# Kernel optimization log

Hardware: AMD Instinct MI355X
Metric: run time of the kernel (lower is better)

The kernel has to match this reference:

```python
import jax, jax.numpy as jnp
import numpy as np

N = 1_000_000          # points
C_IN = 10              # decorated point features
C_OUT = 64             # pillar feature channels
S = 30_000             # number of pillars (segments)
EPS = 1e-3             # BatchNorm1d eps


def setup_inputs() -> dict:
    key = jax.random.key(0)
    ks = jax.random.split(key, 8)
    inputs = jax.random.normal(ks[0], (N, C_IN), dtype=jnp.float32)
    # every pillar gets ~N/S points; sorted, all segments non-empty
    unq_inv = jnp.sort(jnp.arange(N, dtype=jnp.int32) % S)
    W_lin = jax.random.normal(ks[1], (C_OUT, C_IN), dtype=jnp.float32) * 0.3
    gamma = 1.0 + 0.1 * jax.random.normal(ks[2], (C_OUT,), dtype=jnp.float32)
    beta = 0.1 * jax.random.normal(ks[3], (C_OUT,), dtype=jnp.float32)
    dw1 = jax.random.normal(ks[4], (C_OUT,), dtype=jnp.float32) * 0.5      # depthwise 1x1 conv (groups=C)
    pw1 = jax.random.normal(ks[5], (C_OUT, C_OUT), dtype=jnp.float32) * 0.1  # pointwise 1x1 conv
    dw2 = jax.random.normal(ks[6], (C_OUT,), dtype=jnp.float32) * 0.5
    pw2 = jax.random.normal(ks[7], (C_OUT, C_OUT), dtype=jnp.float32) * 0.1
    return {"inputs": inputs, "unq_inv": unq_inv, "W_lin": W_lin,
            "gamma": gamma, "beta": beta, "dw1": dw1, "pw1": pw1,
            "dw2": dw2, "pw2": pw2}


def reference(inputs, unq_inv, W_lin, gamma, beta, dw1, pw1, dw2, pw2):
    # Linear (no bias) -> BN (training-mode batch stats) -> ReLU
    x = inputs @ W_lin.T                                   # [N, C]
    mu = jnp.mean(x, axis=0)
    var = jnp.mean(jnp.square(x - mu), axis=0)             # biased var, as torch BN
    x = (x - mu) * jax.lax.rsqrt(var + EPS) * gamma + beta
    x = jax.nn.relu(x)

    # MAFF attention: local branch (depthwise scale -> swish -> 1x1 conv)
    s = x * dw1                                            # groups=C 1x1 conv == per-channel scale
    xl = (s * jax.nn.sigmoid(s)) @ pw1.T                   # [N, C]
    # global branch: avg-pool over points -> depthwise scale -> relu -> 1x1 conv
    g = jnp.mean(x, axis=0)                                # [C]
    xg = pw2 @ jax.nn.relu(dw2 * g)                        # [C]
    wei = jax.nn.sigmoid(xl + xg)                          # broadcast [N,C] + [C]
    xi = x * (1.0 + wei)

    # segment reductions keyed by pillar id (scatter_max + scatter_sum)
    x_max = jax.ops.segment_max(xi, unq_inv, num_segments=S,
                                indices_are_sorted=True)
    x_sum = jax.ops.segment_sum(xi, unq_inv, num_segments=S,
                                indices_are_sorted=True)
    return x_max + x_sum                                   # [S, C]
```

## Files before the change

### kernel.cpp

```cpp
#include <hip/hip_runtime.h>
#include <math.h>

#define N_PTS   1000000
#define CI      10
#define C       64
#define NSEG    30000
#define BN_EPS  1e-3f
#define FROFF   31104

#define MSTR 7
#define GOFF 512
#define GSTR 8
#define CTRI 961

using f32x4 = __attribute__((ext_vector_type(4))) float;
using s16x8 = __attribute__((ext_vector_type(8))) short;

__device__ inline short f2bf(float x) {
    unsigned u = __float_as_uint(x);
    unsigned r = (u + 0x7fffu + ((u >> 16) & 1u)) >> 16;
    return (short)r;
}
__device__ inline unsigned pack_trunc(float lo, float hi) {
    return (__float_as_uint(hi) & 0xffff0000u) | (__float_as_uint(lo) >> 16);
}
__device__ inline float frcp(float x) { return __builtin_amdgcn_rcpf(x); }
__device__ inline void lds_fence() {
    asm volatile("s_waitcnt lgkmcnt(0)" ::: "memory");
}

struct Rows { float2 r0, r1, r2, r3; };

__global__ void __launch_bounds__(256) k_moments(const float* __restrict__ inp,
                                                 const int* __restrict__ idx,
                                                 float* __restrict__ ws,
                                                 int* __restrict__ starts) {
    const int tid = threadIdx.x;
    const int stride = gridDim.x * blockDim.x;
    float v[65];
#pragma unroll
    for (int k = 0; k < 65; ++k) v[k] = 0.f;

    int p = blockIdx.x * blockDim.x + tid;
    float2 a0, a1, a2, a3, a4;
    int ic = 0, ip = 0;
    auto ld = [&](int qq) {
        const float2* r2 = (const float2*)(inp + (size_t)qq * CI);
        a0 = r2[0]; a1 = r2[1]; a2 = r2[2]; a3 = r2[3]; a4 = r2[4];
        ic = idx[qq]; ip = (qq > 0) ? idx[qq - 1] : ic;
    };
    if (p < N_PTS) ld(p);
    while (p < N_PTS) {
        float r[CI] = {a0.x, a0.y, a1.x, a1.y, a2.x, a2.y, a3.x, a3.y, a4.x, a4.y};
        const int cc = ic, cp = ip, cq = p;
        const int pn = p + stride;
        if (pn < N_PTS) ld(pn);

#pragma unroll
        for (int i = 0; i < CI; ++i) v[i] += r[i];
        int kk = 10;
#pragma unroll
        for (int i = 0; i < CI; ++i)
#pragma unroll
            for (int j = i; j < CI; ++j) { v[kk] = fmaf(r[i], r[j], v[kk]); ++kk; }

        if (cq == 0) starts[0] = 0;
        else if (cp != cc) starts[cc] = cq;
        p = pn;
    }

#pragma unroll
    for (int k = 0; k < 65; ++k) {
#pragma unroll
        for (int off = 32; off >= 1; off >>= 1)
            v[k] += __shfl_xor(v[k], off, 64);
    }
    __shared__ float red[4 * 65];
    const int wv = tid >> 6, ln = tid & 63;
    if (ln == 0) {
#pragma unroll
        for (int k = 0; k < 65; ++k) red[wv * 65 + k] = v[k];
    }
    __syncthreads();
    if (tid < 65)
        atomicAdd(&ws[MSTR * tid],
                  red[tid] + red[65 + tid] + red[130 + tid] + red[195 + tid]);
}

__global__ void __launch_bounds__(256) k_gstats(const float* __restrict__ inp,
                                                const float* __restrict__ W,
                                                const float* __restrict__ gamma,
                                                const float* __restrict__ beta,
                                                const float* __restrict__ dw1,
                                                const float* __restrict__ pw1,
                                                const float* __restrict__ dw2,
                                                const float* __restrict__ pw2,
                                                float* __restrict__ ws) {
    const int tid  = threadIdx.x;
    const int wv   = tid >> 6;
    const int lane = tid & 63;
    const int m = lane & 15;
    const int q = lane >> 4;

    __shared__ float wp[C * CI];
    __shared__ float bsh[C];

    if (tid < C) {
        const int c = tid;
        float w[CI];
#pragma unroll
        for (int i = 0; i < CI; ++i) w[i] = W[c * CI + i];
        const float inv_n = 1.f / (float)N_PTS;

        float mu = 0.f;
#pragma unroll
        for (int i = 0; i < CI; ++i) mu = fmaf(w[i], ws[MSTR * i], mu);
        mu *= inv_n;

        float ex2 = 0.f;
        int kk = 10;
#pragma unroll
        for (int i = 0; i < CI; ++i)
#pragma unroll
            for (int j = i; j < CI; ++j) {
                float mm = ws[MSTR * kk];
                float t = w[i] * w[j] * mm;
                ex2 += (i == j) ? t : 2.f * t;
                ++kk;
            }
        ex2 *= inv_n;

        float var = ex2 - mu * mu;
        float rstd = rsqrtf(var + BN_EPS);
        float a = rstd * gamma[c];
        float b = beta[c] - mu * a;
        bsh[c] = b;
#pragma unroll
        for (int i = 0; i < CI; ++i) wp[c * CI + i] = a * w[i];
    }
    __syncthreads();

    s16x8 wfr[4];
#pragma unroll
    for (int nt = 0; nt < 4; ++nt) {
        s16x8 t;
#pragma unroll
        for (int j = 0; j < 8; ++j) {
            int k = 8 * q + j;
            t[j] = (k < CI) ? f2bf(wp[(nt * 16 + m) * CI + k]) : (short)0;
        }
        wfr[nt] = t;
    }
    float bb[4];
#pragma unroll
    for (int nt = 0; nt < 4; ++nt) bb[nt] = bsh[nt * 16 + m];

    const int wid = blockIdx.x * 4 + wv;
    const int nw  = gridDim.x * 4;
    const int NB  = N_PTS / 16;

    auto loadrows = [&](int pb) -> Rows {
        Rows R;
        R.r0 = R.r1 = R.r2 = R.r3 = make_float2(0.f, 0.f);
        const float* row = inp + (size_t)(pb + m) * CI;
        if (q == 0) {
            R.r0 = *(const float2*)(row);     R.r1 = *(const float2*)(row + 2);
            R.r2 = *(const float2*)(row + 4); R.r3 = *(const float2*)(row + 6);
        } else if (q == 1) {
            R.r0 = *(const float2*)(row + 8);
        }
        return R;
    };

    float sm[4] = {0.f, 0.f, 0.f, 0.f};
    const f32x4 zero = {0.f, 0.f, 0.f, 0.f};

    Rows A  = loadrows(wid * 16);
    Rows Bv = loadrows((wid + nw) * 16);
    for (int b = wid; b < NB; b += nw) {
        Rows L = A; A = Bv;
        if (b + 2 * nw < NB) Bv = loadrows((b + 2 * nw) * 16);

        union { s16x8 v; unsigned u[4]; } t;
        t.v = s16x8{0, 0, 0, 0, 0, 0, 0, 0};
        if (q < 2) t.u[0] = pack_trunc(L.r0.x, L.r0.y);
        if (q == 0) {
            t.u[1] = pack_trunc(L.r1.x, L.r1.y);
            t.u[2] = pack_trunc(L.r2.x, L.r2.y);
            t.u[3] = pack_trunc(L.r3.x, L.r3.y);
        }

#pragma unroll
        for (int nt = 0; nt < 4; ++nt) {
            f32x4 xt = __builtin_amdgcn_mfma_f32_16x16x32_bf16(t.v, wfr[nt], zero, 0, 0, 0);
#pragma unroll
            for (int r = 0; r < 4; ++r)
                sm[nt] += fmaxf(xt[r] + bb[nt], 0.f);
        }
    }

#pragma unroll
    for (int nt = 0; nt < 4; ++nt) {
        sm[nt] += __shfl_xor(sm[nt], 16, 64);
        sm[nt] += __shfl_xor(sm[nt], 32, 64);
    }
    float S = sm[0];
    if (q == 1) S = sm[1];
    if (q == 2) S = sm[2];
    if (q == 3) S = sm[3];

    __shared__ float red[4 * 64];
    red[wv * 64 + lane] = S;
    __syncthreads();
    if (tid < 64)
        atomicAdd(&ws[GOFF + GSTR * tid],
                  red[tid] + red[64 + tid] + red[128 + tid] + red[192 + tid]);

    __shared__ int lastf;
    __syncthreads();
    if (tid == 0) {
        __threadfence();
        int old = atomicAdd((int*)ws + CTRI, 1);
        lastf = (old == (int)gridDim.x - 1);
    }
    __syncthreads();
    if (!lastf) return;
    __threadfence();

    __shared__ float T[C], XG[C];
    const float inv_n = 1.f / (float)N_PTS;
    if (tid < 64)
        T[tid] = fmaxf(dw2[tid] * (ws[GOFF + GSTR * tid] * inv_n), 0.f);
    __syncthreads();
    if (tid < 64) {
        float acc = 0.f;
#pragma unroll
        for (int k = 0; k < C; ++k) acc = fmaf(pw2[tid * C + k], T[k], acc);
        XG[tid] = acc;
    }
    __syncthreads();

    if (tid < 64) {
        float4* FR = (float4*)(ws + FROFF);
        union { float4 f; s16x8 v; } u;

#pragma unroll
        for (int nt = 0; nt < 4; ++nt) {
            s16x8 tt;
#pragma unroll
            for (int j = 0; j < 8; ++j) {
                int k = 8 * q + j;
                tt[j] = (k < CI) ? f2bf(wp[(nt * 16 + m) * CI + k]) : (short)0;
            }
            u.v = tt; FR[nt * 64 + lane] = u.f;
        }
#pragma unroll
        for (int nt = 0; nt < 4; ++nt)
#pragma unroll
            for (int kc = 0; kc < 2; ++kc) {
                const float* src = pw1 + (nt * 16 + m) * C + kc * 32 + q * 8;
                float4 p0 = *(const float4*)src, p1 = *(const float4*)(src + 4);
                s16x8 tt;
                tt[0] = f2bf(p0.x); tt[1] = f2bf(p0.y); tt[2] = f2bf(p0.z); tt[3] = f2bf(p0.w);
                tt[4] = f2bf(p1.x); tt[5] = f2bf(p1.y); tt[6] = f2bf(p1.z); tt[7] = f2bf(p1.w);
                u.v = tt; FR[(4 + nt * 2 + kc) * 64 + lane] = u.f;
            }
        float4 f;
        f.x = bsh[m]; f.y = bsh[16 + m]; f.z = bsh[32 + m]; f.w = bsh[48 + m];
        FR[12 * 64 + lane] = f;
        f.x = dw1[m]; f.y = dw1[16 + m]; f.z = dw1[32 + m]; f.w = dw1[48 + m];
        FR[13 * 64 + lane] = f;
        f.x = XG[m]; f.y = XG[16 + m]; f.z = XG[32 + m]; f.w = XG[48 + m];
        FR[14 * 64 + lane] = f;
    }
}

#define LD2 72
#define TILE2 (16 * LD2)
#define SEGW 2
__global__ void __launch_bounds__(256) k_main(const float* __restrict__ inp,
                                              const float* __restrict__ ws,
                                              const int* __restrict__ starts,
                                              float* __restrict__ out) {
    const int tid  = threadIdx.x;
    const int wv   = tid >> 6;
    const int lane = tid & 63;
    const int m = lane & 15;
    const int q = lane >> 4;
    const f32x4 zero = {0.f, 0.f, 0.f, 0.f};

    const float4* FR = (const float4*)(ws + FROFF);
    union { float4 f; s16x8 v; } u;
    s16x8 wfr[4];
#pragma unroll
    for (int nt = 0; nt < 4; ++nt) { u.f = FR[nt * 64 + lane]; wfr[nt] = u.v; }
    s16x8 bfr[4][2];
#pragma unroll
    for (int nt = 0; nt < 4; ++nt)
#pragma unroll
        for (int kc = 0; kc < 2; ++kc) { u.f = FR[(4 + nt * 2 + kc) * 64 + lane]; bfr[nt][kc] = u.v; }
    const float4 bb4  = FR[12 * 64 + lane];
    const float4 d14  = FR[13 * 64 + lane];
    const float4 xg4  = FR[14 * 64 + lane];
    const float bb[4]  = {bb4.x, bb4.y, bb4.z, bb4.w};
    const float d1v[4] = {d14.x, d14.y, d14.z, d14.w};
    const float xgv[4] = {xg4.x, xg4.y, xg4.z, xg4.w};

    __shared__ short sb16[4][2 * TILE2];
    short* const tbase = sb16[wv];

    const int w  = blockIdx.x * 4 + wv;
    const int s0 = w * SEGW;

    const int start = starts[s0];
    const int st1 = starts[s0 + 1];
    const int st2 = (s0 + 2 < NSEG) ? starts[s0 + 2] : N_PTS;
    const int end_all = st2;

    int cur = s0;
    int end_cur = st1;

    float sm[4]  = {0.f, 0.f, 0.f, 0.f};
    float mxv[4] = {-INFINITY, -INFINITY, -INFINITY, -INFINITY};

    auto flushseg = [&](int s) {
#pragma unroll
        for (int nt = 0; nt < 4; ++nt) {
            sm[nt] += __shfl_xor(sm[nt], 16, 64);
            sm[nt] += __shfl_xor(sm[nt], 32, 64);
            mxv[nt] = fmaxf(mxv[nt], __shfl_xor(mxv[nt], 16, 64));
            mxv[nt] = fmaxf(mxv[nt], __shfl_xor(mxv[nt], 32, 64));
        }
        float S = sm[0], M = mxv[0];
        if (q == 1) { S = sm[1]; M = mxv[1]; }
        if (q == 2) { S = sm[2]; M = mxv[2]; }
        if (q == 3) { S = sm[3]; M = mxv[3]; }
        out[(size_t)s * C + lane] = S + M;
#pragma unroll
        for (int nt = 0; nt < 4; ++nt) { sm[nt] = 0.f; mxv[nt] = -INFINITY; }
    };

    auto loadrows = [&](int pb) -> Rows {
        Rows R;
        R.r0 = R.r1 = R.r2 = R.r3 = make_float2(0.f, 0.f);
        const float* row = inp + (size_t)min(pb + m, N_PTS - 1) * CI;
        if (q == 0) {
            R.r0 = *(const float2*)(row);     R.r1 = *(const float2*)(row + 2);
            R.r2 = *(const float2*)(row + 4); R.r3 = *(const float2*)(row + 6);
        } else if (q == 1) {
            R.r0 = *(const float2*)(row + 8);
        }
        return R;
    };

    Rows A = loadrows(start);
    Rows B = (start + 16 < end_all) ? loadrows(start + 16) : A;

    int tog = 0;
    for (int base = start; base < end_all; base += 16, tog ^= 1) {
        short* const myt = tbase + tog * TILE2;
        Rows L = A;
        A = B;
        if (base + 32 < end_all) B = loadrows(base + 32);

        const int nb = min(16, end_all - base);

        union { s16x8 v; unsigned uu[4]; } t;
        t.v = s16x8{0, 0, 0, 0, 0, 0, 0, 0};
        if (q < 2) t.uu[0] = pack_trunc(L.r0.x, L.r0.y);
        if (q == 0) {
            t.uu[1] = pack_trunc(L.r1.x, L.r1.y);
            t.uu[2] = pack_trunc(L.r2.x, L.r2.y);
            t.uu[3] = pack_trunc(L.r3.x, L.r3.y);
        }

        f32x4 xt[4];
#pragma unroll
        for (int nt = 0; nt < 4; ++nt)
            xt[nt] = __builtin_amdgcn_mfma_f32_16x16x32_bf16(t.v, wfr[nt], zero, 0, 0, 0);

        float xn[4][4];
#pragma unroll
        for (int nt = 0; nt < 4; ++nt)
#pragma unroll
            for (int r = 0; r < 4; ++r) {
                float x = fmaxf(xt[nt][r] + bb[nt], 0.f);
                xn[nt][r] = x;
                float sg = x * d1v[nt];
                float sw = sg * frcp(1.f + __expf(-sg));
                myt[(4 * q + r) * LD2 + nt * 16 + m] =
                    (short)(__float_as_uint(sw) >> 16);
            }
        lds_fence();

        s16x8 av[2];
#pragma unroll
        for (int kc = 0; kc < 2; ++kc)
            av[kc] = *(const s16x8*)(myt + m * LD2 + kc * 32 + q * 8);

        f32x4 xi[4];
#pragma unroll
        for (int nt = 0; nt < 4; ++nt) {
            xi[nt] = __builtin_amdgcn_mfma_f32_16x16x32_bf16(av[0], bfr[nt][0], zero, 0, 0, 0);
            xi[nt] = __builtin_amdgcn_mfma_f32_16x16x32_bf16(av[1], bfr[nt][1], xi[nt], 0, 0, 0);
        }

#pragma unroll
        for (int nt = 0; nt < 4; ++nt)
#pragma unroll
            for (int r = 0; r < 4; ++r) {
                float v   = xi[nt][r] + xgv[nt];
                float wei = frcp(1.f + __expf(-v));
                float x   = xn[nt][r];
                xi[nt][r] = fmaf(x, wei, x);
            }

        const int fin = base + nb;
        if (fin <= end_cur) {
            if (nb == 16) {
#pragma unroll
                for (int nt = 0; nt < 4; ++nt)
#pragma unroll
                    for (int r = 0; r < 4; ++r) {
                        sm[nt] += xi[nt][r];
                        mxv[nt] = fmaxf(mxv[nt], xi[nt][r]);
                    }
            } else {
#pragma unroll
                for (int nt = 0; nt < 4; ++nt)
#pragma unroll
                    for (int r = 0; r < 4; ++r) {
                        bool act = (4 * q + r) < nb;
                        sm[nt] += act ? xi[nt][r] : 0.f;
                        mxv[nt] = fmaxf(mxv[nt], act ? xi[nt][r] : -INFINITY);
                    }
            }
            if (fin == end_cur) { flushseg(cur); ++cur; end_cur = st2; }
        } else {
            const int Bn = end_cur - base;
#pragma unroll
            for (int nt = 0; nt < 4; ++nt)
#pragma unroll
                for (int r = 0; r < 4; ++r) {
                    bool act = (4 * q + r) < Bn;
                    sm[nt] += act ? xi[nt][r] : 0.f;
                    mxv[nt] = fmaxf(mxv[nt], act ? xi[nt][r] : -INFINITY);
                }
            flushseg(cur); ++cur;
#pragma unroll
            for (int nt = 0; nt < 4; ++nt)
#pragma unroll
                for (int r = 0; r < 4; ++r) {
                    int pt = 4 * q + r;
                    bool act = (pt >= Bn) && (pt < nb);
                    sm[nt] += act ? xi[nt][r] : 0.f;
                    mxv[nt] = fmaxf(mxv[nt], act ? xi[nt][r] : -INFINITY);
                }
            end_cur = st2;
        }
    }
}

extern "C" void kernel_launch(void* const* d_in, const int* in_sizes, int n_in,
                              void* d_out, int out_size, void* d_ws, size_t ws_size,
                              hipStream_t stream) {
    const float* inp   = (const float*)d_in[0];
    const int*   unq   = (const int*)d_in[1];
    const float* W     = (const float*)d_in[2];
    const float* gamma = (const float*)d_in[3];
    const float* beta  = (const float*)d_in[4];
    const float* dw1   = (const float*)d_in[5];
    const float* pw1   = (const float*)d_in[6];
    const float* dw2   = (const float*)d_in[7];
    const float* pw2   = (const float*)d_in[8];
    float* out = (float*)d_out;
    float* ws  = (float*)d_ws;
    int* starts = (int*)ws + 1024;

    hipMemsetAsync(ws, 0, 1024 * sizeof(float), stream);

    k_moments <<<1024, 256, 0, stream>>>(inp, unq, ws, starts);
    k_gstats  <<<1024, 256, 0, stream>>>(inp, W, gamma, beta, dw1, pw1, dw2, pw2, ws);
    k_main    <<<3750, 256, 0, stream>>>(inp, ws, starts, out);
}
```

Measured before the change: 282.7 us.

## Stage gstats input in LDS with scalar FMA; shrink main kernel blocks

k_gstats now copies a 500-point tile of the input into shared memory and computes the per-channel global mean with scalar FP32 FMAs, one channel per lane, instead of a grid-stride bf16 MFMA loop. Its grid goes from 1024 to 2000 blocks. k_main moves from 256 to 128 threads per block and from a double-buffered bf16 LDS tile to a single fp32 tile, packing to bf16 at read time, which needs an extra LDS fence. This trades MFMA throughput and buffering for simpler code and more, smaller blocks. The scalar path also does more ALU work per point.

```diff
diff --git a/kernel.cpp b/kernel.cpp
--- a/kernel.cpp
+++ b/kernel.cpp
@@ -87,6 +87,7 @@
                   red[tid] + red[65 + tid] + red[130 + tid] + red[195 + tid]);
 }
 
+#define GS_TP 500
 __global__ void __launch_bounds__(256) k_gstats(const float* __restrict__ inp,
                                                 const float* __restrict__ W,
                                                 const float* __restrict__ gamma,
@@ -101,22 +102,28 @@
     const int lane = tid & 63;
     const int m = lane & 15;
     const int q = lane >> 4;
-
+    const float inv_n = 1.f / (float)N_PTS;
+
+    __shared__ float tile[GS_TP * CI];
     __shared__ float wp[C * CI];
     __shared__ float bsh[C];
-
-    if (tid < C) {
-        const int c = tid;
+    __shared__ float red[4 * 64];
+
+    {
+        const float4* src = (const float4*)(inp + (size_t)blockIdx.x * GS_TP * CI);
+        float4* dst = (float4*)tile;
+        for (int i = tid; i < GS_TP * CI / 4; i += 256) dst[i] = src[i];
+    }
+
+    float wa[CI], b;
+    {
         float w[CI];
 #pragma unroll
-        for (int i = 0; i < CI; ++i) w[i] = W[c * CI + i];
-        const float inv_n = 1.f / (float)N_PTS;
-
+        for (int i = 0; i < CI; ++i) w[i] = W[lane * CI + i];
         float mu = 0.f;
 #pragma unroll
         for (int i = 0; i < CI; ++i) mu = fmaf(w[i], ws[MSTR * i], mu);
         mu *= inv_n;
-
         float ex2 = 0.f;
         int kk = 10;
 #pragma unroll
@@ -129,88 +136,48 @@
                 ++kk;
             }
         ex2 *= inv_n;
-
         float var = ex2 - mu * mu;
         float rstd = rsqrtf(var + BN_EPS);
-        float a = rstd * gamma[c];
-        float b = beta[c] - mu * a;
-        bsh[c] = b;
-#pragma unroll
-        for (int i = 0; i < CI; ++i) wp[c * CI + i] = a * w[i];
-    }
-    __syncthreads();
-
-    s16x8 wfr[4];
-#pragma unroll
-    for (int nt = 0; nt < 4; ++nt) {
-        s16x8 t;
-#pragma unroll
-        for (int j = 0; j < 8; ++j) {
-            int k = 8 * q + j;
-            t[j] = (k < CI) ? f2bf(wp[(nt * 16 + m) * CI + k]) : (short)0;
-        }
-        wfr[nt] = t;
-    }
-    float bb[4];
-#pragma unroll
-    for (int nt = 0; nt < 4; ++nt) bb[nt] = bsh[nt * 16 + m];
-
-    const int wid = blockIdx.x * 4 + wv;
-    const int nw  = gridDim.x * 4;
-    const int NB  = N_PTS / 16;
-
-    auto loadrows = [&](int pb) -> Rows {
-        Rows R;
-        R.r0 = R.r1 = R.r2 = R.r3 = make_float2(0.f, 0.f);
-        const float* row = inp + (size_t)(pb + m) * CI;
-        if (q == 0) {
-            R.r0 = *(const float2*)(row);     R.r1 = *(const float2*)(row + 2);
-            R.r2 = *(const float2*)(row + 4); R.r3 = *(const float2*)(row + 6);
-        } else if (q == 1) {
-            R.r0 = *(const float2*)(row + 8);
-        }
-        return R;
-    };
-
-    float sm[4] = {0.f, 0.f, 0.f, 0.f};
-    const f32x4 zero = {0.f, 0.f, 0.f, 0.f};
-
-    Rows A  = loadrows(wid * 16);
-    Rows Bv = loadrows((wid + nw) * 16);
-    for (int b = wid; b < NB; b += nw) {
-        Rows L = A; A = Bv;
-        if (b + 2 * nw < NB) Bv = loadrows((b + 2 * nw) * 16);
-
-        union { s16x8 v; unsigned u[4]; } t;
-        t.v = s16x8{0, 0, 0, 0, 0, 0, 0, 0};
-        if (q < 2) t.u[0] = pack_trunc(L.r0.x, L.r0.y);
-        if (q == 0) {
-            t.u[1] = pack_trunc(L.r1.x, L.r1.y);
-            t.u[2] = pack_trunc(L.r2.x, L.r2.y);
-            t.u[3] = pack_trunc(L.r3.x, L.r3.y);
-        }
-
-#pragma unroll
-        for (int nt = 0; nt < 4; ++nt) {
-            f32x4 xt = __builtin_amdgcn_mfma_f32_16x16x32_bf16(t.v, wfr[nt], zero, 0, 0, 0);
-#pragma unroll
-            for (int r = 0; r < 4; ++r)
-                sm[nt] += fmaxf(xt[r] + bb[nt], 0.f);
-        }
-    }
-
-#pragma unroll
-    for (int nt = 0; nt < 4; ++nt) {
-        sm[nt] += __shfl_xor(sm[nt], 16, 64);
-        sm[nt] += __shfl_xor(sm[nt], 32, 64);
-    }
-    float S = sm[0];
-    if (q == 1) S = sm[1];
-    if (q == 2) S = sm[2];
-    if (q == 3) S = sm[3];
-
-    __shared__ float red[4 * 64];
-    red[wv * 64 + lane] = S;
+        float a = rstd * gamma[lane];
+        b = beta[lane] - mu * a;
+#pragma unroll
+        for (int i = 0; i < CI; ++i) wa[i] = a * w[i];
+        if (wv == 0) {
+            bsh[lane] = b;
+#pragma unroll
+            for (int i = 0; i < CI; ++i) wp[lane * CI + i] = wa[i];
+        }
+    }
+    __syncthreads();
+
+    float g0 = 0.f, g1 = 0.f;
+    const int ps = wv * 125;
+    for (int p = ps; p < ps + 124; p += 2) {
+        const float* r0 = &tile[p * CI];
+        const float* r1 = &tile[(p + 1) * CI];
+        float acc0 = b, acc1 = b;
+#pragma unroll
+        for (int i2 = 0; i2 < 5; ++i2) {
+            float2 u0 = *(const float2*)(r0 + 2 * i2);
+            float2 u1 = *(const float2*)(r1 + 2 * i2);
+            acc0 = fmaf(wa[2 * i2], u0.x, fmaf(wa[2 * i2 + 1], u0.y, acc0));
+            acc1 = fmaf(wa[2 * i2], u1.x, fmaf(wa[2 * i2 + 1], u1.y, acc1));
+        }
+        g0 += fmaxf(acc0, 0.f);
+        g1 += fmaxf(acc1, 0.f);
+    }
+    {
+        const float* r0 = &tile[(ps + 124) * CI];
+        float acc0 = b;
+#pragma unroll
+        for (int i2 = 0; i2 < 5; ++i2) {
+            float2 u0 = *(const float2*)(r0 + 2 * i2);
+            acc0 = fmaf(wa[2 * i2], u0.x, fmaf(wa[2 * i2 + 1], u0.y, acc0));
+        }
+        g0 += fmaxf(acc0, 0.f);
+    }
+
+    red[wv * 64 + lane] = g0 + g1;
     __syncthreads();
     if (tid < 64)
         atomicAdd(&ws[GOFF + GSTR * tid],
@@ -228,7 +195,6 @@
     __threadfence();
 
     __shared__ float T[C], XG[C];
-    const float inv_n = 1.f / (float)N_PTS;
     if (tid < 64)
         T[tid] = fmaxf(dw2[tid] * (ws[GOFF + GSTR * tid] * inv_n), 0.f);
     __syncthreads();
@@ -275,10 +241,9 @@
     }
 }
 
-#define LD2 72
-#define TILE2 (16 * LD2)
+#define LD 68
 #define SEGW 2
-__global__ void __launch_bounds__(256) k_main(const float* __restrict__ inp,
+__global__ void __launch_bounds__(128) k_main(const float* __restrict__ inp,
                                               const float* __restrict__ ws,
                                               const int* __restrict__ starts,
                                               float* __restrict__ out) {
@@ -306,15 +271,15 @@
     const float d1v[4] = {d14.x, d14.y, d14.z, d14.w};
     const float xgv[4] = {xg4.x, xg4.y, xg4.z, xg4.w};
 
-    __shared__ short sb16[4][2 * TILE2];
-    short* const tbase = sb16[wv];
-
-    const int w  = blockIdx.x * 4 + wv;
+    __shared__ float sb[2][16 * LD];
+    float* my = sb[wv];
+
+    const int w  = blockIdx.x * 2 + wv;
     const int s0 = w * SEGW;
 
-    const int start = starts[s0];
-    const int st1 = starts[s0 + 1];
-    const int st2 = (s0 + 2 < NSEG) ? starts[s0 + 2] : N_PTS;
+    int st1 = starts[s0 + 1];
+    int st2 = (s0 + 2 < NSEG) ? starts[s0 + 2] : N_PTS;
+    const int start   = starts[s0];
     const int end_all = st2;
 
     int cur = s0;
@@ -356,9 +321,7 @@
     Rows A = loadrows(start);
     Rows B = (start + 16 < end_all) ? loadrows(start + 16) : A;
 
-    int tog = 0;
-    for (int base = start; base < end_all; base += 16, tog ^= 1) {
-        short* const myt = tbase + tog * TILE2;
+    for (int base = start; base < end_all; base += 16) {
         Rows L = A;
         A = B;
         if (base + 32 < end_all) B = loadrows(base + 32);
@@ -388,15 +351,23 @@
                 xn[nt][r] = x;
                 float sg = x * d1v[nt];
                 float sw = sg * frcp(1.f + __expf(-sg));
-                myt[(4 * q + r) * LD2 + nt * 16 + m] =
-                    (short)(__float_as_uint(sw) >> 16);
+                my[(4 * q + r) * LD + nt * 16 + m] = sw;
             }
         lds_fence();
 
         s16x8 av[2];
 #pragma unroll
-        for (int kc = 0; kc < 2; ++kc)
-            av[kc] = *(const s16x8*)(myt + m * LD2 + kc * 32 + q * 8);
+        for (int kc = 0; kc < 2; ++kc) {
+            const float* src = &my[m * LD + kc * 32 + q * 8];
+            float4 p0 = *(const float4*)src;
+            float4 p1 = *(const float4*)(src + 4);
+            union { s16x8 v; unsigned uu[4]; } tt;
+            tt.uu[0] = pack_trunc(p0.x, p0.y);
+            tt.uu[1] = pack_trunc(p0.z, p0.w);
+            tt.uu[2] = pack_trunc(p1.x, p1.y);
+            tt.uu[3] = pack_trunc(p1.z, p1.w);
+            av[kc] = tt.v;
+        }
 
         f32x4 xi[4];
 #pragma unroll
@@ -404,6 +375,7 @@
             xi[nt] = __builtin_amdgcn_mfma_f32_16x16x32_bf16(av[0], bfr[nt][0], zero, 0, 0, 0);
             xi[nt] = __builtin_amdgcn_mfma_f32_16x16x32_bf16(av[1], bfr[nt][1], xi[nt], 0, 0, 0);
         }
+        lds_fence();
 
 #pragma unroll
         for (int nt = 0; nt < 4; ++nt)
@@ -437,12 +409,12 @@
             }
             if (fin == end_cur) { flushseg(cur); ++cur; end_cur = st2; }
         } else {
-            const int Bn = end_cur - base;
+            const int B = end_cur - base;
 #pragma unroll
             for (int nt = 0; nt < 4; ++nt)
 #pragma unroll
                 for (int r = 0; r < 4; ++r) {
-                    bool act = (4 * q + r) < Bn;
+                    bool act = (4 * q + r) < B;
                     sm[nt] += act ? xi[nt][r] : 0.f;
                     mxv[nt] = fmaxf(mxv[nt], act ? xi[nt][r] : -INFINITY);
                 }
@@ -452,7 +424,7 @@
 #pragma unroll
                 for (int r = 0; r < 4; ++r) {
                     int pt = 4 * q + r;
-                    bool act = (pt >= Bn) && (pt < nb);
+                    bool act = (pt >= B) && (pt < nb);
                     sm[nt] += act ? xi[nt][r] : 0.f;
                     mxv[nt] = fmaxf(mxv[nt], act ? xi[nt][r] : -INFINITY);
                 }
@@ -480,6 +452,6 @@
     hipMemsetAsync(ws, 0, 1024 * sizeof(float), stream);
 
     k_moments <<<1024, 256, 0, stream>>>(inp, unq, ws, starts);
-    k_gstats  <<<1024, 256, 0, stream>>>(inp, W, gamma, beta, dw1, pw1, dw2, pw2, ws);
-    k_main    <<<3750, 256, 0, stream>>>(inp, ws, starts, out);
-}
+    k_gstats  <<<2000, 256, 0, stream>>>(inp, W, gamma, beta, dw1, pw1, dw2, pw2, ws);
+    k_main    <<<7500, 128, 0, stream>>>(inp, ws, starts, out);
+}
```

Measured after the change: 298.2 us. +5.5%, slower.
